# Kernel optimization log

Hardware: AMD Instinct MI355X
Metric: run time of the kernel (lower is better)

The kernel has to match this reference:

```python
import jax, jax.numpy as jnp
import numpy as np

EPS = 1e-6


def _make_coord_3d(D, H, W, dtype):
    # torch make_coord_3d(flatten=False).permute(3,0,1,2): channels stacked as (x, y, z)
    lz = jnp.linspace(-1.0, 1.0, D, dtype=dtype)
    ly = jnp.linspace(-1.0, 1.0, H, dtype=dtype)
    lx = jnp.linspace(-1.0, 1.0, W, dtype=dtype)
    cz, cy, cx = jnp.meshgrid(lz, ly, lx, indexing='ij')
    return jnp.stack([cx, cy, cz], axis=0)  # [3, D, H, W]


def _trilinear_border(vol, gd, gh, gw):
    # vol: [C, D, H, W]; gd/gh/gw: [Q] normalized coords for the D/H/W axes.
    # Matches torch grid_sample(mode='bilinear', align_corners=False, padding_mode='border').
    C, D, H, W = vol.shape
    z = (gd + 1.0) * (D * 0.5) - 0.5
    y = (gh + 1.0) * (H * 0.5) - 0.5
    x = (gw + 1.0) * (W * 0.5) - 0.5
    z0 = jnp.floor(z); y0 = jnp.floor(y); x0 = jnp.floor(x)
    wz = (z - z0)[None]; wy = (y - y0)[None]; wx = (x - x0)[None]  # [1, Q]
    z0i = jnp.clip(z0.astype(jnp.int32), 0, D - 1); z1i = jnp.clip(z0.astype(jnp.int32) + 1, 0, D - 1)
    y0i = jnp.clip(y0.astype(jnp.int32), 0, H - 1); y1i = jnp.clip(y0.astype(jnp.int32) + 1, 0, H - 1)
    x0i = jnp.clip(x0.astype(jnp.int32), 0, W - 1); x1i = jnp.clip(x0.astype(jnp.int32) + 1, 0, W - 1)
    g = lambda zi, yi, xi: vol[:, zi, yi, xi]  # gather -> [C, Q]
    return (g(z0i, y0i, x0i) * (1 - wz) * (1 - wy) * (1 - wx)
            + g(z0i, y0i, x1i) * (1 - wz) * (1 - wy) * wx
            + g(z0i, y1i, x0i) * (1 - wz) * wy * (1 - wx)
            + g(z0i, y1i, x1i) * (1 - wz) * wy * wx
            + g(z1i, y0i, x0i) * wz * (1 - wy) * (1 - wx)
            + g(z1i, y0i, x1i) * wz * (1 - wy) * wx
            + g(z1i, y1i, x0i) * wz * wy * (1 - wx)
            + g(z1i, y1i, x1i) * wz * wy * wx)


def _forward(inp, coord, cell, W0, b0, W1, b1, W2, b2, W3, b3):
    feat = inp  # identity encoder: inp is the latent feature grid
    B, C, D, H, W = feat.shape
    rx = 2.0 / D / 2.0; ry = 2.0 / H / 2.0; rz = 2.0 / W / 2.0
    sizes = jnp.array([D, H, W], dtype=feat.dtype)
    feat_coord = _make_coord_3d(D, H, W, feat.dtype)  # [3, D, H, W]
    sample_b = jax.vmap(_trilinear_border, in_axes=(0, 0, 0, 0))
    sample_c = jax.vmap(_trilinear_border, in_axes=(None, 0, 0, 0))

    rel_cell = cell * sizes  # [B, Q, 3]
    cell_vol = jnp.abs(cell[..., 0] * cell[..., 1] * cell[..., 2])
    scale_sq = jnp.clip(8.0 / (cell_vol + 1e-8), 1.0, 64.0)[..., None]  # [B, Q, 1]

    def mlp(x):
        h = jax.nn.relu(x @ W0 + b0)
        h = jax.nn.relu(h @ W1 + b1)
        h = jax.nn.relu(h @ W2 + b2)
        return h @ W3 + b3

    preds, areas = [], []
    for vx in (-1, 1):
        for vy in (-1, 1):
            for vz in (-1, 1):
                shift = jnp.array([vx * rx + EPS, vy * ry + EPS, vz * rz + EPS], dtype=coord.dtype)
                c = jnp.clip(coord + shift, -1.0 + 1e-6, 1.0 - 1e-6)
                gd, gh, gw = c[..., 0], c[..., 1], c[..., 2]
                q_feat = sample_b(feat, gd, gh, gw).transpose(0, 2, 1)        # [B, Q, C]
                q_coord = sample_c(feat_coord, gd, gh, gw).transpose(0, 2, 1)  # [B, Q, 3]
                rel_coord = (coord - q_coord) * sizes
                x = jnp.concatenate([q_feat, rel_coord, rel_cell, scale_sq], axis=-1)
                preds.append(mlp(x))  # [B, Q, 1]
                areas.append(jnp.abs(rel_coord[..., 0] * rel_coord[..., 1] * rel_coord[..., 2]) + 1e-9)
    tot_area = jnp.stack(areas).sum(axis=0)
    areas = areas[::-1]  # local-ensemble diagonal-swap of areas
    ret = sum(p * (a / tot_area)[..., None] for p, a in zip(preds, areas))
    return ret


def setup_inputs() -> dict:
    key = jax.random.key(0)
    ks = jax.random.split(key, 8)
    B, C, D, Q, HID = 1, 64, 32, 131072, 256
    in_dim = C + 3 + 3 + 1  # 71
    w = lambda k, shape, fan_in: jax.random.normal(k, shape, jnp.float32) * (1.0 / np.sqrt(fan_in))
    inp = jax.random.normal(ks[0], (B, C, D, D, D), jnp.float32)
    coord = jax.random.uniform(ks[1], (B, Q, 3), jnp.float32, -1.0, 1.0)
    cell = jnp.full((B, Q, 3), 2.0 / 64.0, jnp.float32)  # uniform cell size of a 64^3 query grid
    return {
        'inp': inp, 'coord': coord, 'cell': cell,
        'W0': w(ks[2], (in_dim, HID), in_dim), 'b0': jnp.zeros((HID,), jnp.float32),
        'W1': w(ks[3], (HID, HID), HID), 'b1': jnp.zeros((HID,), jnp.float32),
        'W2': w(ks[4], (HID, HID), HID), 'b2': jnp.zeros((HID,), jnp.float32),
        'W3': w(ks[5], (HID, 1), HID), 'b3': jnp.zeros((1,), jnp.float32),
    }


def reference(inp, coord, cell, W0, b0, W1, b1, W2, b2, W3, b3):
    return _forward(inp, coord, cell, W0, b0, W1, b1, W2, b2, W3, b3)
```

## Files before the change

### kernel.cpp

```cpp
#include <hip/hip_runtime.h>

typedef __attribute__((ext_vector_type(8))) short s16x8;
typedef __attribute__((ext_vector_type(4))) float f32x4;

__device__ __forceinline__ unsigned short f2bf(float x) {
  unsigned u = __float_as_uint(x);
  u = (u + 0x7fffu + ((u >> 16) & 1u)) >> 16;
  return (unsigned short)u;
}
__device__ __forceinline__ unsigned cvt_pk_bf16(float a, float b) {
  unsigned r;
  asm("v_cvt_pk_bf16_f32 %0, %1, %2" : "=v"(r) : "v"(a), "v"(b));
  return r;
}
__device__ __forceinline__ float bflo(unsigned v) { return __uint_as_float(v << 16); }
__device__ __forceinline__ float bfhi(unsigned v) { return __uint_as_float(v & 0xffff0000u); }

__device__ __forceinline__ void lgkm_barrier() {
  asm volatile("s_waitcnt lgkmcnt(0)" ::: "memory");
  __builtin_amdgcn_s_barrier();
  asm volatile("" ::: "memory");
}

#define FEAT_OFF 0
#define W0F_OFF  2097152
#define W1F_OFF  (W0F_OFF + 24576)
#define W2F_OFF  (W1F_OFF + 65536)
#define W3P_OFF  (W2F_OFF + 65536)
#define WS_TOTAL (W3P_OFF + 512)

__device__ __forceinline__ int col_log(int kp) {
  return (kp & 0xC0) | ((kp & 3) << 4) | ((kp >> 2) & 15);
}

__global__ void liif_prep(const float* __restrict__ inp,
                          const float* __restrict__ W0,
                          const float* __restrict__ W1,
                          const float* __restrict__ W2,
                          const float* __restrict__ W3,
                          unsigned short* __restrict__ ws) {
  int tid = blockIdx.x * 256 + threadIdx.x;
  if (tid < 2097152) {
    int pos = tid >> 6, c = tid & 63;
    ws[FEAT_OFF + tid] = f2bf(inp[c * 32768 + pos]);
  } else if (tid < W1F_OFF) {
    int e = tid - W0F_OFF;
    int j = e & 7, L = (e >> 3) & 63, nt = (e >> 9) & 15, c = e >> 13;
    int k = c * 32 + (L >> 4) * 8 + j, n = nt * 16 + (L & 15);
    ws[tid] = (k < 71) ? f2bf(W0[k * 256 + n]) : (unsigned short)0;
  } else if (tid < W2F_OFF) {
    int e = tid - W1F_OFF;
    int j = e & 7, L = (e >> 3) & 63, nt = (e >> 9) & 15, c = e >> 13;
    int kp = c * 32 + (L >> 4) * 8 + j, n = nt * 16 + (L & 15);
    ws[tid] = f2bf(W1[col_log(kp) * 256 + n]);
  } else if (tid < W3P_OFF) {
    int e = tid - W2F_OFF;
    int j = e & 7, L = (e >> 3) & 63, nt = (e >> 9) & 15, c = e >> 13;
    int kp = c * 32 + (L >> 4) * 8 + j, n = nt * 16 + (L & 15);
    ws[tid] = f2bf(W2[col_log(kp) * 256 + n]);
  } else if (tid < W3P_OFF + 256) {
    int e = tid - W3P_OFF;
    float* w3p = (float*)(ws + W3P_OFF);
    w3p[e] = W3[col_log(e)];
  }
}

template<int KC, bool PRE>
__device__ __forceinline__ void run_layer(const unsigned short* __restrict__ Wf,
                                          const float* __restrict__ bias,
                                          const unsigned short* A, int astride,
                                          unsigned short* H,
                                          const unsigned short* __restrict__ Wnext,
                                          s16x8 (&nb)[4],
                                          int wave, int quad, int l16, int lane) {
  float bv[4];
#pragma unroll
  for (int ntl = 0; ntl < 4; ++ntl) bv[ntl] = bias[(wave * 4 + ntl) * 16 + l16];

  f32x4 acc[4][4];
#pragma unroll
  for (int i = 0; i < 4; ++i)
#pragma unroll
    for (int j = 0; j < 4; ++j) acc[i][j] = (f32x4){0.f, 0.f, 0.f, 0.f};

  __builtin_amdgcn_s_setprio(1);
#pragma unroll
  for (int c = 0; c < KC; ++c) {
    s16x8 a[4];
#pragma unroll
    for (int rt = 0; rt < 4; ++rt)
      a[rt] = *(const s16x8*)(A + (rt * 16 + l16) * astride + c * 32 + quad * 8);
#pragma unroll
    for (int ntl = 0; ntl < 4; ++ntl) {
      int nt = wave * 4 + ntl;
      s16x8 b = (c == 0) ? nb[ntl]
                         : *(const s16x8*)(Wf + (((c * 16 + nt) * 64 + lane) << 3));
#pragma unroll
      for (int rt = 0; rt < 4; ++rt)
        acc[rt][ntl] = __builtin_amdgcn_mfma_f32_16x16x32_bf16(a[rt], b, acc[rt][ntl], 0, 0, 0);
    }
  }
  __builtin_amdgcn_s_setprio(0);

  if constexpr (PRE) {
#pragma unroll
    for (int ntl = 0; ntl < 4; ++ntl)
      nb[ntl] = *(const s16x8*)(Wnext + (((wave * 4 + ntl) * 64 + lane) << 3));
  }

  lgkm_barrier();

  const int cbase = wave * 64 + l16 * 4;
#pragma unroll
  for (int rt = 0; rt < 4; ++rt) {
#pragma unroll
    for (int i = 0; i < 4; ++i) {
      float v0 = fmaxf(acc[rt][0][i] + bv[0], 0.0f);
      float v1 = fmaxf(acc[rt][1][i] + bv[1], 0.0f);
      float v2 = fmaxf(acc[rt][2][i] + bv[2], 0.0f);
      float v3 = fmaxf(acc[rt][3][i] + bv[3], 0.0f);
      int r = rt * 16 + quad * 4 + i;
      uint2 pw = make_uint2(cvt_pk_bf16(v0, v1), cvt_pk_bf16(v2, v3));
      *(uint2*)(H + r * 264 + cbase) = pw;
    }
  }
  lgkm_barrier();
}

__global__ __launch_bounds__(256, 4)
void liif_main(const float* __restrict__ coord,
               const float* __restrict__ cell,
               const float* __restrict__ b0,
               const float* __restrict__ b1,
               const float* __restrict__ b2,
               const float* __restrict__ b3,
               const unsigned short* __restrict__ ws,
               float* __restrict__ out) {
  __shared__ __align__(16) unsigned short sm_h[64 * 264];
  __shared__ float sm_area[64];
  __shared__ float sm_pred[64];
  unsigned short* sm_x = sm_h;

  const unsigned short* feat = ws + FEAT_OFF;
  const int tid = threadIdx.x;
  const int lane = tid & 63;
  const int wave = tid >> 6;
  const int quad = lane >> 4;
  const int l16 = lane & 15;

  s16x8 nb[4];
#pragma unroll
  for (int ntl = 0; ntl < 4; ++ntl)
    nb[ntl] = *(const s16x8*)(ws + W0F_OFF + (((wave * 4 + ntl) * 64 + lane) << 3));

  {
    const int row = tid >> 2, p = tid & 3;
    const int ql = row >> 3, s = row & 7;
    const int q = blockIdx.x * 8 + ql;
    const float c0r = coord[q * 3 + 0], c1r = coord[q * 3 + 1], c2r = coord[q * 3 + 2];
    const float R = 0.03125f;
    const float sh0 = ((s & 4) ? R : -R) + 1e-6f;
    const float sh1 = ((s & 2) ? R : -R) + 1e-6f;
    const float sh2 = ((s & 1) ? R : -R) + 1e-6f;
    const float LO = -1.0f + 1e-6f, HI = 1.0f - 1e-6f;
    float c0 = fminf(fmaxf(c0r + sh0, LO), HI);
    float c1 = fminf(fmaxf(c1r + sh1, LO), HI);
    float c2 = fminf(fmaxf(c2r + sh2, LO), HI);
    float z = (c0 + 1.0f) * 16.0f - 0.5f;
    float y = (c1 + 1.0f) * 16.0f - 0.5f;
    float x = (c2 + 1.0f) * 16.0f - 0.5f;
    float zf = floorf(z), yf = floorf(y), xf = floorf(x);
    float wz = z - zf, wy = y - yf, wx = x - xf;
    int z0 = min(max((int)zf, 0), 31), z1 = min(max((int)zf + 1, 0), 31);
    int y0 = min(max((int)yf, 0), 31), y1 = min(max((int)yf + 1, 0), 31);
    int x0 = min(max((int)xf, 0), 31), x1 = min(max((int)xf + 1, 0), 31);
    float wz0 = 1.0f - wz, wy0 = 1.0f - wy, wx0 = 1.0f - wx;

    float w[8] = { wz0 * wy0 * wx0, wz0 * wy0 * wx, wz0 * wy * wx0, wz0 * wy * wx,
                   wz  * wy0 * wx0, wz  * wy0 * wx, wz  * wy * wx0, wz  * wy * wx };
    int idx[8] = { (z0 * 32 + y0) * 32 + x0, (z0 * 32 + y0) * 32 + x1,
                   (z0 * 32 + y1) * 32 + x0, (z0 * 32 + y1) * 32 + x1,
                   (z1 * 32 + y0) * 32 + x0, (z1 * 32 + y0) * 32 + x1,
                   (z1 * 32 + y1) * 32 + x0, (z1 * 32 + y1) * 32 + x1 };

    float acc[16];
#pragma unroll
    for (int i = 0; i < 16; ++i) acc[i] = 0.0f;
#pragma unroll
    for (int corner = 0; corner < 8; ++corner) {
      const uint4* cp = (const uint4*)(feat + idx[corner] * 64 + p * 16);
      uint4 v0 = cp[0], v1 = cp[1];
      float wc = w[corner];
      unsigned vv[8] = { v0.x, v0.y, v0.z, v0.w, v1.x, v1.y, v1.z, v1.w };
#pragma unroll
      for (int d = 0; d < 8; ++d) {
        acc[2 * d]     += wc * bflo(vv[d]);
        acc[2 * d + 1] += wc * bfhi(vv[d]);
      }
    }
    unsigned pw[8];
#pragma unroll
    for (int d = 0; d < 8; ++d)
      pw[d] = cvt_pk_bf16(acc[2 * d], acc[2 * d + 1]);
    uint4* dst = (uint4*)(&sm_x[row * 104 + p * 16]);
    dst[0] = make_uint4(pw[0], pw[1], pw[2], pw[3]);
    dst[1] = make_uint4(pw[4], pw[5], pw[6], pw[7]);

    if (p == 0) {
      const float step = 2.0f / 31.0f;
      float qc0 = wx0 * (-1.0f + step * x0) + wx * (-1.0f + step * x1);
      float qc1 = wy0 * (-1.0f + step * y0) + wy * (-1.0f + step * y1);
      float qc2 = wz0 * (-1.0f + step * z0) + wz * (-1.0f + step * z1);
      float rel0 = (c0r - qc0) * 32.0f;
      float rel1 = (c1r - qc1) * 32.0f;
      float rel2 = (c2r - qc2) * 32.0f;
      sm_area[row] = fabsf(rel0 * rel1 * rel2) + 1e-9f;
      float cl0 = cell[q * 3 + 0], cl1 = cell[q * 3 + 1], cl2 = cell[q * 3 + 2];
      float ssq = fminf(fmaxf(8.0f / (fabsf(cl0 * cl1 * cl2) + 1e-8f), 1.0f), 64.0f);
      unsigned tw0 = cvt_pk_bf16(rel0, rel1);
      unsigned tw1 = cvt_pk_bf16(rel2, cl0 * 32.0f);
      unsigned tw2 = cvt_pk_bf16(cl1 * 32.0f, cl2 * 32.0f);
      unsigned tw3 = cvt_pk_bf16(ssq, 0.0f);
      uint4* d2 = (uint4*)(&sm_x[row * 104 + 64]);
      d2[0] = make_uint4(tw0, tw1, tw2, tw3);
      d2[1] = make_uint4(0, 0, 0, 0);
      d2[2] = make_uint4(0, 0, 0, 0);
      d2[3] = make_uint4(0, 0, 0, 0);
    }
  }
  lgkm_barrier();

  run_layer<3, true >(ws + W0F_OFF, b0, sm_x, 104, sm_h, ws + W1F_OFF, nb, wave, quad, l16, lane);
  run_layer<8, true >(ws + W1F_OFF, b1, sm_h, 264, sm_h, ws + W2F_OFF, nb, wave, quad, l16, lane);
  run_layer<8, false>(ws + W2F_OFF, b2, sm_h, 264, sm_h, nullptr,      nb, wave, quad, l16, lane);

  {
    const int row = tid >> 2, p = tid & 3;
    const unsigned short* hp = sm_h + row * 264 + p * 64;
    const float* W3p = (const float*)(ws + W3P_OFF);
    float sum = 0.0f;
#pragma unroll
    for (int kk = 0; kk < 8; ++kk) {
      const uint4 v = *(const uint4*)(hp + kk * 8);
      const float4 wa = *(const float4*)(W3p + p * 64 + kk * 8);
      const float4 wb = *(const float4*)(W3p + p * 64 + kk * 8 + 4);
      sum += wa.x * bflo(v.x) + wa.y * bfhi(v.x);
      sum += wa.z * bflo(v.y) + wa.w * bfhi(v.y);
      sum += wb.x * bflo(v.z) + wb.y * bfhi(v.z);
      sum += wb.z * bflo(v.w) + wb.w * bfhi(v.w);
    }
    sum += __shfl_xor(sum, 1);
    sum += __shfl_xor(sum, 2);
    if (p == 0) sm_pred[row] = sum + b3[0];
  }
  lgkm_barrier();

  if (tid < 8) {
    const int ql = tid;
    float tot = 0.0f, ret = 0.0f;
#pragma unroll
    for (int s = 0; s < 8; ++s) tot += sm_area[ql * 8 + s];
#pragma unroll
    for (int s = 0; s < 8; ++s) ret += sm_pred[ql * 8 + s] * sm_area[ql * 8 + (7 - s)];
    out[blockIdx.x * 8 + ql] = ret / tot;
  }
}

extern "C" void kernel_launch(void* const* d_in, const int* in_sizes, int n_in,
                              void* d_out, int out_size, void* d_ws, size_t ws_size,
                              hipStream_t stream) {
  const float* inp   = (const float*)d_in[0];
  const float* coord = (const float*)d_in[1];
  const float* cell  = (const float*)d_in[2];
  const float* W0    = (const float*)d_in[3];
  const float* b0    = (const float*)d_in[4];
  const float* W1    = (const float*)d_in[5];
  const float* b1    = (const float*)d_in[6];
  const float* W2    = (const float*)d_in[7];
  const float* b2    = (const float*)d_in[8];
  const float* W3    = (const float*)d_in[9];
  const float* b3    = (const float*)d_in[10];
  unsigned short* ws = (unsigned short*)d_ws;
  float* out = (float*)d_out;

  const int Q = in_sizes[1] / 3;
  hipLaunchKernelGGL(liif_prep, dim3((WS_TOTAL + 255) / 256), dim3(256), 0, stream,
                     inp, W0, W1, W2, W3, ws);
  hipLaunchKernelGGL(liif_main, dim3(Q / 8), dim3(256), 0, stream,
                     coord, cell, b0, b1, b2, b3, ws, out);
}
```

Before: 439.8 us.

## Prefetch MFMA weight fragments three K-steps ahead across layers

Weight B-fragments for the three MLP layers are now held in a 3-deep register ring buffer indexed across all 19 K-steps, so each step's global load is issued three steps before use instead of just before the MFMA. The trilinear gather is split so all 16 corner loads are issued before any accumulation, exposing memory-level parallelism. Launch bounds drop from 4 to 2 blocks per CU to give room for the extra registers, which may lower occupancy.

Result: slower. 471.4 us (+7.2%).

```diff
diff --git a/kernel.cpp b/kernel.cpp
--- a/kernel.cpp
+++ b/kernel.cpp
@@ -28,6 +28,12 @@
 #define W2F_OFF  (W1F_OFF + 65536)
 #define W3P_OFF  (W2F_OFF + 65536)
 #define WS_TOTAL (W3P_OFF + 512)
+
+__host__ __device__ constexpr int STEP_OFF(int s) {
+  return s < 3 ? W0F_OFF + s * 8192
+       : s < 11 ? W1F_OFF + (s - 3) * 8192
+                : W2F_OFF + (s - 11) * 8192;
+}
 
 __device__ __forceinline__ int col_log(int kp) {
   return (kp & 0xC0) | ((kp & 3) << 4) | ((kp >> 2) & 15);
@@ -65,13 +71,12 @@
   }
 }
 
-template<int KC, bool PRE>
-__device__ __forceinline__ void run_layer(const unsigned short* __restrict__ Wf,
-                                          const float* __restrict__ bias,
+template<int KC, int SBASE>
+__device__ __forceinline__ void run_layer(const float* __restrict__ bias,
                                           const unsigned short* A, int astride,
                                           unsigned short* H,
-                                          const unsigned short* __restrict__ Wnext,
-                                          s16x8 (&nb)[4],
+                                          const unsigned short* __restrict__ ws, int bofs,
+                                          s16x8 (&bb)[3][4],
                                           int wave, int quad, int l16, int lane) {
   float bv[4];
 #pragma unroll
@@ -92,21 +97,19 @@
       a[rt] = *(const s16x8*)(A + (rt * 16 + l16) * astride + c * 32 + quad * 8);
 #pragma unroll
     for (int ntl = 0; ntl < 4; ++ntl) {
-      int nt = wave * 4 + ntl;
-      s16x8 b = (c == 0) ? nb[ntl]
-                         : *(const s16x8*)(Wf + (((c * 16 + nt) * 64 + lane) << 3));
 #pragma unroll
       for (int rt = 0; rt < 4; ++rt)
-        acc[rt][ntl] = __builtin_amdgcn_mfma_f32_16x16x32_bf16(a[rt], b, acc[rt][ntl], 0, 0, 0);
+        acc[rt][ntl] = __builtin_amdgcn_mfma_f32_16x16x32_bf16(
+            a[rt], bb[(SBASE + c) % 3][ntl], acc[rt][ntl], 0, 0, 0);
+    }
+    if (SBASE + c + 3 < 19) {
+#pragma unroll
+      for (int ntl = 0; ntl < 4; ++ntl)
+        bb[(SBASE + c) % 3][ntl] =
+            *(const s16x8*)(ws + STEP_OFF(SBASE + c + 3) + bofs + ntl * 512);
     }
   }
   __builtin_amdgcn_s_setprio(0);
-
-  if constexpr (PRE) {
-#pragma unroll
-    for (int ntl = 0; ntl < 4; ++ntl)
-      nb[ntl] = *(const s16x8*)(Wnext + (((wave * 4 + ntl) * 64 + lane) << 3));
-  }
 
   lgkm_barrier();
 
@@ -127,7 +130,7 @@
   lgkm_barrier();
 }
 
-__global__ __launch_bounds__(256, 4)
+__global__ __launch_bounds__(256, 2)
 void liif_main(const float* __restrict__ coord,
                const float* __restrict__ cell,
                const float* __restrict__ b0,
@@ -148,10 +151,13 @@
   const int quad = lane >> 4;
   const int l16 = lane & 15;
 
-  s16x8 nb[4];
-#pragma unroll
-  for (int ntl = 0; ntl < 4; ++ntl)
-    nb[ntl] = *(const s16x8*)(ws + W0F_OFF + (((wave * 4 + ntl) * 64 + lane) << 3));
+  const int bofs = wave * 2048 + lane * 8;
+  s16x8 bb[3][4];
+#pragma unroll
+  for (int s = 0; s < 3; ++s)
+#pragma unroll
+    for (int ntl = 0; ntl < 4; ++ntl)
+      bb[s][ntl] = *(const s16x8*)(ws + STEP_OFF(s) + bofs + ntl * 512);
 
   {
     const int row = tid >> 2, p = tid & 3;
@@ -183,15 +189,23 @@
                    (z1 * 32 + y0) * 32 + x0, (z1 * 32 + y0) * 32 + x1,
                    (z1 * 32 + y1) * 32 + x0, (z1 * 32 + y1) * 32 + x1 };
 
-    float acc[16];
-#pragma unroll
-    for (int i = 0; i < 16; ++i) acc[i] = 0.0f;
+    uint4 u[16];
 #pragma unroll
     for (int corner = 0; corner < 8; ++corner) {
       const uint4* cp = (const uint4*)(feat + idx[corner] * 64 + p * 16);
-      uint4 v0 = cp[0], v1 = cp[1];
+      u[2 * corner] = cp[0];
+      u[2 * corner + 1] = cp[1];
+    }
+
+    float acc[16];
+#pragma unroll
+    for (int i = 0; i < 16; ++i) acc[i] = 0.0f;
+#pragma unroll
+    for (int corner = 0; corner < 8; ++corner) {
       float wc = w[corner];
-      unsigned vv[8] = { v0.x, v0.y, v0.z, v0.w, v1.x, v1.y, v1.z, v1.w };
+      unsigned vv[8] = { u[2 * corner].x, u[2 * corner].y, u[2 * corner].z, u[2 * corner].w,
+                         u[2 * corner + 1].x, u[2 * corner + 1].y,
+                         u[2 * corner + 1].z, u[2 * corner + 1].w };
 #pragma unroll
       for (int d = 0; d < 8; ++d) {
         acc[2 * d]     += wc * bflo(vv[d]);
@@ -230,9 +244,9 @@
   }
   lgkm_barrier();
 
-  run_layer<3, true >(ws + W0F_OFF, b0, sm_x, 104, sm_h, ws + W1F_OFF, nb, wave, quad, l16, lane);
-  run_layer<8, true >(ws + W1F_OFF, b1, sm_h, 264, sm_h, ws + W2F_OFF, nb, wave, quad, l16, lane);
-  run_layer<8, false>(ws + W2F_OFF, b2, sm_h, 264, sm_h, nullptr,      nb, wave, quad, l16, lane);
+  run_layer<3, 0 >(b0, sm_x, 104, sm_h, ws, bofs, bb, wave, quad, l16, lane);
+  run_layer<8, 3 >(b1, sm_h, 264, sm_h, ws, bofs, bb, wave, quad, l16, lane);
+  run_layer<8, 11>(b2, sm_h, 264, sm_h, ws, bofs, bb, wave, quad, l16, lane);
 
   {
     const int row = tid >> 2, p = tid & 3;
```
